# Kernel optimization log

Measured on AMD Instinct MI355X. Metric: run time of the kernel, lower is better.

## Reference

```python
import jax, jax.numpy as jnp
import numpy as np

N = 50000      # nodes
E = 800000     # edges (avg degree 16)
D = 128        # d_model
H = 8          # num_heads
DK = D // H    # d_k = 16


def setup_inputs() -> dict:
    key = jax.random.key(0)
    ks = jax.random.split(key, 9)
    scale = np.float32(1.0 / np.sqrt(D))
    return {
        "q": jax.random.normal(ks[0], (N, D), jnp.float32),
        "k": jax.random.normal(ks[1], (N, D), jnp.float32),
        "v": jax.random.normal(ks[2], (N, D), jnp.float32),
        "e": jax.random.normal(ks[3], (E, D), jnp.float32),
        "src": jax.random.randint(ks[4], (E,), 0, N),
        "dst": jax.random.randint(ks[5], (E,), 0, N),
        # nn.Linear(D, D, bias=False) weights, stored as [in, out]
        "Wq": jax.random.normal(ks[6], (D, D), jnp.float32) * scale,
        "Wk": jax.random.normal(ks[7], (D, D), jnp.float32) * scale,
        "Wv": jax.random.normal(ks[8], (D, D), jnp.float32) * scale,
    }


def reference(q, k, v, e, src, dst, Wq, Wk, Wv):
    inv_sqrt_dk = np.float32(1.0 / np.sqrt(DK))
    # node-level V projection, then per-edge gather of src V  -> [E, H, DK]
    Vn = (v @ Wv).reshape(N, H, DK)
    Ve = Vn[src]
    # per-edge Q from dst node, K from (src k + edge feature e)
    Qe = (q[dst] @ Wq).reshape(E, H, DK)
    Ke = ((k[src] + e) @ Wk).reshape(E, H, DK)
    # per-edge HxH score matrix: Q @ K^T / sqrt(d_k), leaky-relu
    s = jnp.einsum("ehd,egd->ehg", Qe, Ke) * inv_sqrt_dk   # [E, H, H]
    s = jax.nn.leaky_relu(s)
    # softmax over last head axis (within each edge, as in reduce_func dim=-1)
    A = jax.nn.softmax(s, axis=-1)
    # per-edge message, heads regrouped -> [E, D]
    He = jnp.einsum("ehg,egd->ehd", A, Ve).reshape(E, D)
    # plain sum over incoming edges per destination node -> [N, D]
    return jax.ops.segment_sum(He, dst, num_segments=N)
```

## Files before the change

kernel.cpp:

```cpp
#include <hip/hip_runtime.h>
#include <hip/hip_bf16.h>
#include <math.h>

#define NN 50000
#define EE 800000
#define DD 128
#define HH 8
#define DKK 16

typedef __attribute__((ext_vector_type(8))) short short8;
typedef __attribute__((ext_vector_type(4))) float f32x4;
typedef __attribute__((ext_vector_type(4))) unsigned short ushort4v;
typedef __attribute__((ext_vector_type(8))) unsigned short ushort8v;

static __device__ __forceinline__ unsigned short f2bf(float x) {
  __hip_bfloat16 h = __float2bfloat16(x);
  return *reinterpret_cast<unsigned short*>(&h);
}
static __device__ __forceinline__ float bf2f(unsigned short u) {
  return __uint_as_float(((unsigned int)u) << 16);
}

__global__ __launch_bounds__(256) void hist_kernel(const int* __restrict__ dst,
                                                   int* __restrict__ cnt) {
  int i4 = blockIdx.x * 256 + threadIdx.x;
  if (i4 < EE / 4) {
    int4 d = *(const int4*)&dst[i4 * 4];
    atomicAdd(&cnt[d.x], 1);
    atomicAdd(&cnt[d.y], 1);
    atomicAdd(&cnt[d.z], 1);
    atomicAdd(&cnt[d.w], 1);
  }
}

#define SCAN_NB ((NN + 1023) / 1024)

__global__ __launch_bounds__(256) void scan1_kernel(const int* __restrict__ cnt,
                                                    int* __restrict__ bsum) {
  __shared__ int red[256];
  const int b = blockIdx.x, t = threadIdx.x;
  const int base = b * 1024 + t * 4;
  int s = 0;
  if (base + 3 < NN) {
    int4 v = *(const int4*)&cnt[base];
    s = v.x + v.y + v.z + v.w;
  } else {
    for (int j = 0; j < 4; ++j) if (base + j < NN) s += cnt[base + j];
  }
  red[t] = s;
  __syncthreads();
  for (int off = 1; off < 256; off <<= 1) {
    int v = (t >= off) ? red[t - off] : 0;
    __syncthreads();
    red[t] += v;
    __syncthreads();
  }
  if (t == 255) bsum[b] = red[255];
}

__global__ __launch_bounds__(64) void scan2_kernel(const int* __restrict__ bsum,
                                                   int* __restrict__ bpre) {
  int t = threadIdx.x;
  int v = (t < SCAN_NB) ? bsum[t] : 0;
  for (int off = 1; off < 64; off <<= 1) {
    int u = __shfl_up(v, off);
    if (t >= off) v += u;
  }
  if (t < SCAN_NB) bpre[t + 1] = v;
  if (t == 0) bpre[0] = 0;
}

__global__ __launch_bounds__(256) void scan3_kernel(const int* __restrict__ cnt,
                                                    const int* __restrict__ bpre,
                                                    int* __restrict__ rowptr) {
  __shared__ int red[256];
  const int b = blockIdx.x, t = threadIdx.x;
  const int base = b * 1024 + t * 4;
  int v0 = 0, v1 = 0, v2 = 0, v3 = 0;
  if (base + 3 < NN) {
    int4 v = *(const int4*)&cnt[base];
    v0 = v.x; v1 = v.y; v2 = v.z; v3 = v.w;
  } else {
    if (base + 0 < NN) v0 = cnt[base + 0];
    if (base + 1 < NN) v1 = cnt[base + 1];
    if (base + 2 < NN) v2 = cnt[base + 2];
    if (base + 3 < NN) v3 = cnt[base + 3];
  }
  red[t] = v0 + v1 + v2 + v3;
  __syncthreads();
  for (int off = 1; off < 256; off <<= 1) {
    int v = (t >= off) ? red[t - off] : 0;
    __syncthreads();
    red[t] += v;
    __syncthreads();
  }
  int r = bpre[b] + ((t == 0) ? 0 : red[t - 1]);
  if (base + 0 < NN) { rowptr[base + 0] = r; r += v0; }
  if (base + 1 < NN) { rowptr[base + 1] = r; r += v1; }
  if (base + 2 < NN) { rowptr[base + 2] = r; r += v2; }
  if (base + 3 < NN) { rowptr[base + 3] = r; }
}

__global__ __launch_bounds__(256) void fill_kernel(const int* __restrict__ dst,
                                                   const int* __restrict__ rowptr,
                                                   int* __restrict__ cur,
                                                   int* __restrict__ perm) {
  int i4 = blockIdx.x * 256 + threadIdx.x;
  if (i4 < EE / 4) {
    int4 dv = *(const int4*)&dst[i4 * 4];
    int d0 = dv.x, d1 = dv.y, d2 = dv.z, d3 = dv.w;
    int s0 = atomicAdd(&cur[d0], 1); perm[rowptr[d0] + s0] = i4 * 4 + 0;
    int s1 = atomicAdd(&cur[d1], 1); perm[rowptr[d1] + s1] = i4 * 4 + 1;
    int s2 = atomicAdd(&cur[d2], 1); perm[rowptr[d2] + s2] = i4 * 4 + 2;
    int s3 = atomicAdd(&cur[d3], 1); perm[rowptr[d3] + s3] = i4 * 4 + 3;
  }
}

__global__ void prep_w_kernel(const float* __restrict__ Wq,
                              const float* __restrict__ Wk,
                              const float* __restrict__ Wv,
                              unsigned short* __restrict__ WqT,
                              unsigned short* __restrict__ WkT,
                              unsigned short* __restrict__ WvT) {
  int c = blockIdx.x & 127;
  int m = blockIdx.x >> 7;
  int j = threadIdx.x;
  const float* W = (m == 0) ? Wq : (m == 1) ? Wk : Wv;
  unsigned short* o = (m == 0) ? WqT : (m == 1) ? WkT : WvT;
  o[j * DD + c] = f2bf(W[c * DD + j]);
}

__global__ __launch_bounds__(512) void node_proj_kernel(
    const float* __restrict__ q, const float* __restrict__ v,
    const float* __restrict__ k,
    const unsigned short* __restrict__ WqT, const unsigned short* __restrict__ WvT,
    unsigned short* __restrict__ Qh, unsigned short* __restrict__ Vh,
    unsigned short* __restrict__ kh)
{
  __shared__ __align__(16) unsigned short xl[64 * 136];
  const int tid = threadIdx.x;
  const int n0 = blockIdx.x * 64;

  #pragma unroll
  for (int p = 0; p < 2; ++p) {
    int f = p * 512 + tid;
    int i = f >> 4, c8 = f & 15;
    int n = n0 + i;
    if (n < NN) {
      float4 a = *(const float4*)&k[(size_t)n * DD + c8 * 8];
      float4 b = *(const float4*)&k[(size_t)n * DD + c8 * 8 + 4];
      ushort8v o = { f2bf(a.x), f2bf(a.y), f2bf(a.z), f2bf(a.w),
                     f2bf(b.x), f2bf(b.y), f2bf(b.z), f2bf(b.w) };
      *(ushort8v*)&kh[(size_t)n * DD + c8 * 8] = o;
    }
  }

  for (int m = 0; m < 2; ++m) {
    const float* x = m ? v : q;
    const unsigned short* WT = m ? WvT : WqT;
    unsigned short* o = m ? Vh : Qh;

    __syncthreads();
    #pragma unroll
    for (int p = 0; p < 4; ++p) {
      int f = p * 512 + tid;
      int i = f >> 5, c4 = f & 31;
      int n = n0 + i;
      float4 t = (n < NN) ? *(const float4*)&x[(size_t)n * DD + c4 * 4]
                          : float4{0.f, 0.f, 0.f, 0.f};
      ushort4v u = { f2bf(t.x), f2bf(t.y), f2bf(t.z), f2bf(t.w) };
      *(ushort4v*)&xl[i * 136 + c4 * 4] = u;
    }
    __syncthreads();

    const int lane = tid & 63, wid = tid >> 6;
    const int rg = wid & 3, cg = wid >> 2;
    const int lr = lane & 15, lg = lane >> 4;

    f32x4 acc0 = {0.f,0.f,0.f,0.f}, acc1 = {0.f,0.f,0.f,0.f};
    f32x4 acc2 = {0.f,0.f,0.f,0.f}, acc3 = {0.f,0.f,0.f,0.f};

    const unsigned short* Ab = &xl[(rg * 16 + lr) * 136];
    const unsigned short* B0 = &WT[(size_t)(cg * 64 +  0 + lr) * DD];
    const unsigned short* B1 = &WT[(size_t)(cg * 64 + 16 + lr) * DD];
    const unsigned short* B2 = &WT[(size_t)(cg * 64 + 32 + lr) * DD];
    const unsigned short* B3 = &WT[(size_t)(cg * 64 + 48 + lr) * DD];

    #pragma unroll
    for (int kk = 0; kk < 4; ++kk) {
      const int kof = kk * 32 + lg * 8;
      short8 a = *(const short8*)(Ab + kof);
      acc0 = __builtin_amdgcn_mfma_f32_16x16x32_bf16(a, *(const short8*)(B0 + kof), acc0, 0, 0, 0);
      acc1 = __builtin_amdgcn_mfma_f32_16x16x32_bf16(a, *(const short8*)(B1 + kof), acc1, 0, 0, 0);
      acc2 = __builtin_amdgcn_mfma_f32_16x16x32_bf16(a, *(const short8*)(B2 + kof), acc2, 0, 0, 0);
      acc3 = __builtin_amdgcn_mfma_f32_16x16x32_bf16(a, *(const short8*)(B3 + kof), acc3, 0, 0, 0);
    }

    const int r0 = rg * 16 + lg * 4;
    const int cb = cg * 64 + lr;
    #pragma unroll
    for (int r = 0; r < 4; ++r) {
      int n = n0 + r0 + r;
      if (n < NN) {
        unsigned short* orow = &o[(size_t)n * DD + cb];
        orow[ 0] = f2bf(acc0[r]);
        orow[16] = f2bf(acc1[r]);
        orow[32] = f2bf(acc2[r]);
        orow[48] = f2bf(acc3[r]);
      }
    }
  }
}

__global__ __launch_bounds__(512) void edge_attn_kernel(
    const unsigned short* __restrict__ kh, const float* __restrict__ e,
    const int* __restrict__ src, const int* __restrict__ dst,
    const int* __restrict__ perm,
    const unsigned short* __restrict__ WkT,
    const unsigned short* __restrict__ Qh, const unsigned short* __restrict__ Vh,
    float* __restrict__ out)
{
  __shared__ __align__(16) unsigned short buf[128 * 136];
  __shared__ __align__(16) unsigned short vbuf[128 * 136];
  __shared__ __align__(16) unsigned short pbuf[8 * 16 * 24];
  __shared__ int s_perm[128], s_src[128], s_dst[128];

  const int tid = threadIdx.x;
  const size_t e0 = (size_t)blockIdx.x * 128;

  if (tid < 128) {
    int pe = perm[e0 + tid];
    s_perm[tid] = pe;
    s_src[tid] = src[pe];
    s_dst[tid] = dst[pe];
  }
  __syncthreads();

  #pragma unroll
  for (int p = 0; p < 4; ++p) {
    int f = p * 512 + tid;
    int i2 = f >> 4, c8 = f & 15;
    *(ushort8v*)&vbuf[i2 * 136 + c8 * 8] =
        *(const ushort8v*)&Vh[(size_t)s_src[i2] * DD + c8 * 8];
  }

  #pragma unroll
  for (int p = 0; p < 4; ++p) {
    int f = p * 512 + tid;
    int i2 = f >> 4, c8 = f & 15;
    ushort8v kv = *(const ushort8v*)&kh[(size_t)s_src[i2] * DD + c8 * 8];
    float4 ea = *(const float4*)&e[(size_t)s_perm[i2] * DD + c8 * 8];
    float4 eb = *(const float4*)&e[(size_t)s_perm[i2] * DD + c8 * 8 + 4];
    ushort8v o;
    o[0] = f2bf(bf2f(kv[0]) + ea.x);
    o[1] = f2bf(bf2f(kv[1]) + ea.y);
    o[2] = f2bf(bf2f(kv[2]) + ea.z);
    o[3] = f2bf(bf2f(kv[3]) + ea.w);
    o[4] = f2bf(bf2f(kv[4]) + eb.x);
    o[5] = f2bf(bf2f(kv[5]) + eb.y);
    o[6] = f2bf(bf2f(kv[6]) + eb.z);
    o[7] = f2bf(bf2f(kv[7]) + eb.w);
    *(ushort8v*)&buf[i2 * 136 + c8 * 8] = o;
  }
  __syncthreads();

  const int lane = tid & 63, wid = tid >> 6;
  const int lr = lane & 15, lg = lane >> 4;

  {
    const int rgA = wid & 3, rgB = (wid & 3) + 4, cg = wid >> 2;

    f32x4 aA0 = {0.f,0.f,0.f,0.f}, aA1 = {0.f,0.f,0.f,0.f};
    f32x4 aA2 = {0.f,0.f,0.f,0.f}, aA3 = {0.f,0.f,0.f,0.f};
    f32x4 aB0 = {0.f,0.f,0.f,0.f}, aB1 = {0.f,0.f,0.f,0.f};
    f32x4 aB2 = {0.f,0.f,0.f,0.f}, aB3 = {0.f,0.f,0.f,0.f};

    const unsigned short* AbA = &buf[(rgA * 16 + lr) * 136];
    const unsigned short* AbB = &buf[(rgB * 16 + lr) * 136];
    const unsigned short* B0 = &WkT[(size_t)(cg * 64 +  0 + lr) * DD];
    const unsigned short* B1 = &WkT[(size_t)(cg * 64 + 16 + lr) * DD];
    const unsigned short* B2 = &WkT[(size_t)(cg * 64 + 32 + lr) * DD];
    const unsigned short* B3 = &WkT[(size_t)(cg * 64 + 48 + lr) * DD];

    #pragma unroll
    for (int kk = 0; kk < 4; ++kk) {
      const int kof = kk * 32 + lg * 8;
      short8 b0 = *(const short8*)(B0 + kof);
      short8 b1 = *(const short8*)(B1 + kof);
      short8 b2 = *(const short8*)(B2 + kof);
      short8 b3 = *(const short8*)(B3 + kof);
      short8 fA = *(const short8*)(AbA + kof);
      short8 fB = *(const short8*)(AbB + kof);
      aA0 = __builtin_amdgcn_mfma_f32_16x16x32_bf16(fA, b0, aA0, 0, 0, 0);
      aA1 = __builtin_amdgcn_mfma_f32_16x16x32_bf16(fA, b1, aA1, 0, 0, 0);
      aA2 = __builtin_amdgcn_mfma_f32_16x16x32_bf16(fA, b2, aA2, 0, 0, 0);
      aA3 = __builtin_amdgcn_mfma_f32_16x16x32_bf16(fA, b3, aA3, 0, 0, 0);
      aB0 = __builtin_amdgcn_mfma_f32_16x16x32_bf16(fB, b0, aB0, 0, 0, 0);
      aB1 = __builtin_amdgcn_mfma_f32_16x16x32_bf16(fB, b1, aB1, 0, 0, 0);
      aB2 = __builtin_amdgcn_mfma_f32_16x16x32_bf16(fB, b2, aB2, 0, 0, 0);
      aB3 = __builtin_amdgcn_mfma_f32_16x16x32_bf16(fB, b3, aB3, 0, 0, 0);
    }

    __syncthreads();

    const int rA = rgA * 16 + lg * 4;
    const int rB = rgB * 16 + lg * 4;
    const int cb = cg * 64 + lr;
    #pragma unroll
    for (int r = 0; r < 4; ++r) {
      buf[(rA + r) * 136 + cb +  0] = f2bf(aA0[r]);
      buf[(rA + r) * 136 + cb + 16] = f2bf(aA1[r]);
      buf[(rA + r) * 136 + cb + 32] = f2bf(aA2[r]);
      buf[(rA + r) * 136 + cb + 48] = f2bf(aA3[r]);
      buf[(rB + r) * 136 + cb +  0] = f2bf(aB0[r]);
      buf[(rB + r) * 136 + cb + 16] = f2bf(aB1[r]);
      buf[(rB + r) * 136 + cb + 32] = f2bf(aB2[r]);
      buf[(rB + r) * 136 + cb + 48] = f2bf(aB3[r]);
    }
  }
  __syncthreads();

  {
    const int ebase = wid * 16;
    const bool valid = ((lr < 8) == (lg < 2));
    unsigned short* pb = &pbuf[wid * 16 * 24];
    const short8 zero8 = {0, 0, 0, 0, 0, 0, 0, 0};

    short8 qf[8];
    #pragma unroll
    for (int j = 0; j < 8; ++j) {
      if (lg < 2) {
        int ie = ebase + 2 * j + (lr >> 3);
        qf[j] = *(const short8*)&Qh[(size_t)s_dst[ie] * DD + (lr & 7) * DKK + lg * 8];
      } else qf[j] = zero8;
    }

    #pragma unroll
    for (int j = 0; j < 8; ++j) {
      const int iea = ebase + 2 * j, ieb = iea + 1;

      short8 af = zero8;
      if (lg < 2) {
        int ie = (lr < 8) ? iea : ieb;
        af = *(const short8*)&buf[ie * 136 + (lr & 7) * DKK + lg * 8];
      }
      f32x4 c = {0.f, 0.f, 0.f, 0.f};
      c = __builtin_amdgcn_mfma_f32_16x16x32_bf16(af, qf[j], c, 0, 0, 0);

      float s0, s1, s2, s3;
      {
        float x0 = c[0] * 0.25f, x1 = c[1] * 0.25f;
        float x2 = c[2] * 0.25f, x3 = c[3] * 0.25f;
        x0 = (x0 >= 0.f) ? x0 : 0.01f * x0;
        x1 = (x1 >= 0.f) ? x1 : 0.01f * x1;
        x2 = (x2 >= 0.f) ? x2 : 0.01f * x2;
        x3 = (x3 >= 0.f) ? x3 : 0.01f * x3;
        s0 = valid ? x0 : -1e30f;
        s1 = valid ? x1 : -1e30f;
        s2 = valid ? x2 : -1e30f;
        s3 = valid ? x3 : -1e30f;
      }
      float m = fmaxf(fmaxf(s0, s1), fmaxf(s2, s3));
      m = fmaxf(m, __shfl_xor(m, 16));
      m = fmaxf(m, __shfl_xor(m, 32));
      float p0 = __expf(s0 - m), p1 = __expf(s1 - m);
      float p2 = __expf(s2 - m), p3 = __expf(s3 - m);
      float su = p0 + p1 + p2 + p3;
      su += __shfl_xor(su, 16);
      su += __shfl_xor(su, 32);
      float rs = 1.0f / su;

      ushort4v pk = { f2bf(p0 * rs), f2bf(p1 * rs), f2bf(p2 * rs), f2bf(p3 * rs) };
      *(ushort4v*)&pb[lr * 24 + lg * 4] = pk;

      short8 pa = zero8;
      if (lg < 2) pa = *(const short8*)&pb[lr * 24 + lg * 8];
      short8 vf = zero8;
      if (lg < 2) {
        const unsigned short* vr = &vbuf[(lg ? ieb : iea) * 136 + lr];
        vf[0] = (short)vr[0 * 16];
        vf[1] = (short)vr[1 * 16];
        vf[2] = (short)vr[2 * 16];
        vf[3] = (short)vr[3 * 16];
        vf[4] = (short)vr[4 * 16];
        vf[5] = (short)vr[5 * 16];
        vf[6] = (short)vr[6 * 16];
        vf[7] = (short)vr[7 * 16];
      }
      f32x4 hc = {0.f, 0.f, 0.f, 0.f};
      hc = __builtin_amdgcn_mfma_f32_16x16x32_bf16(pa, vf, hc, 0, 0, 0);

      #pragma unroll
      for (int r = 0; r < 4; ++r) {
        int rr = lg * 4 + r;
        int ie = (rr < 8) ? iea : ieb;
        buf[ie * 136 + (rr & 7) * DKK + lr] = f2bf(hc[r]);
      }
    }
  }

  {
    const int c = tid >> 6, d2 = tid & 63;
    const int base = c * 16;
    float s0 = 0.0f, s1 = 0.0f;
    int curd = s_dst[base];
    #pragma unroll 8
    for (int j = 0; j < 16; ++j) {
      int i2 = base + j;
      int dn2 = s_dst[i2];
      if (dn2 != curd) {
        atomicAdd(&out[(size_t)curd * DD + d2 * 2],     s0);
        atomicAdd(&out[(size_t)curd * DD + d2 * 2 + 1], s1);
        s0 = 0.0f; s1 = 0.0f;
        curd = dn2;
      }
      unsigned int w = *(const unsigned int*)&buf[i2 * 136 + d2 * 2];
      s0 += bf2f((unsigned short)(w & 0xffff));
      s1 += bf2f((unsigned short)(w >> 16));
    }
    atomicAdd(&out[(size_t)curd * DD + d2 * 2],     s0);
    atomicAdd(&out[(size_t)curd * DD + d2 * 2 + 1], s1);
  }
}

extern "C" void kernel_launch(void* const* d_in, const int* in_sizes, int n_in,
                              void* d_out, int out_size, void* d_ws, size_t ws_size,
                              hipStream_t stream) {
  const float* q  = (const float*)d_in[0];
  const float* k  = (const float*)d_in[1];
  const float* v  = (const float*)d_in[2];
  const float* e  = (const float*)d_in[3];
  const int*   src = (const int*)d_in[4];
  const int*   dst = (const int*)d_in[5];
  const float* Wq = (const float*)d_in[6];
  const float* Wk = (const float*)d_in[7];
  const float* Wv = (const float*)d_in[8];

  float* out = (float*)d_out;
  char* wsb = (char*)d_ws;
  unsigned short* Qh  = (unsigned short*)wsb;
  unsigned short* Vh  = Qh + (size_t)NN * DD;
  unsigned short* kh  = Vh + (size_t)NN * DD;
  unsigned short* WqT = kh + (size_t)NN * DD;
  unsigned short* WkT = WqT + DD * DD;
  unsigned short* WvT = WkT + DD * DD;
  int* cnt    = (int*)(WvT + DD * DD);
  int* cur    = cnt + NN;
  int* rowptr = cur + NN;
  int* bsum   = rowptr + NN + 1;
  int* bpre   = bsum + 64;
  int* perm   = bpre + 64;

  hipMemsetAsync(d_out, 0, (size_t)NN * DD * sizeof(float), stream);
  hipMemsetAsync(cnt, 0, 2 * NN * sizeof(int), stream);

  hist_kernel <<<(EE / 4 + 255) / 256, 256, 0, stream>>>(dst, cnt);
  scan1_kernel<<<SCAN_NB, 256, 0, stream>>>(cnt, bsum);
  scan2_kernel<<<1, 64, 0, stream>>>(bsum, bpre);
  scan3_kernel<<<SCAN_NB, 256, 0, stream>>>(cnt, bpre, rowptr);
  fill_kernel <<<(EE / 4 + 255) / 256, 256, 0, stream>>>(dst, rowptr, cur, perm);

  prep_w_kernel<<<3 * DD, DD, 0, stream>>>(Wq, Wk, Wv, WqT, WkT, WvT);
  node_proj_kernel<<<(NN + 63) / 64, 512, 0, stream>>>(q, v, k, WqT, WvT,
                                                       Qh, Vh, kh);
  edge_attn_kernel<<<EE / 128, 512, 0, stream>>>(kh, e, src, dst, perm,
                                                 WkT, Qh, Vh, out);
}
```

Before: 387.3 us.

## Make edge attention kernel wave-private to eliminate block-wide barriers

Restructures the edge attention kernel so each wavefront owns 16 edges end to end: it loads its own indices, gathers K+e and V rows into a private LDS slice, does the full 16x128 Wk projection itself with 8 MFMA accumulators, and then runs attention and aggregation. This removes all __syncthreads calls and the cross-wave split of the projection GEMM, so waves no longer wait on each other. The LDS row padding is also dropped from 136 to 128, which can cause bank conflicts on the strided column accesses. Each wave now reads all of WkT from global or cache instead of a quarter, and it relies on wave-level ordering of LDS writes and reads without explicit barriers.

New measurement: 475.1 us. 1.23x slower.

```diff
diff --git a/kernel.cpp b/kernel.cpp
--- a/kernel.cpp
+++ b/kernel.cpp
@@ -220,37 +220,41 @@
     const unsigned short* __restrict__ Qh, const unsigned short* __restrict__ Vh,
     float* __restrict__ out)
 {
-  __shared__ __align__(16) unsigned short buf[128 * 136];
-  __shared__ __align__(16) unsigned short vbuf[128 * 136];
+  __shared__ __align__(16) unsigned short buf[128 * 128];
+  __shared__ __align__(16) unsigned short vbuf[128 * 128];
   __shared__ __align__(16) unsigned short pbuf[8 * 16 * 24];
   __shared__ int s_perm[128], s_src[128], s_dst[128];
 
   const int tid = threadIdx.x;
-  const size_t e0 = (size_t)blockIdx.x * 128;
-
-  if (tid < 128) {
-    int pe = perm[e0 + tid];
-    s_perm[tid] = pe;
-    s_src[tid] = src[pe];
-    s_dst[tid] = dst[pe];
-  }
-  __syncthreads();
+  const int lane = tid & 63, wid = tid >> 6;
+  const int lr = lane & 15, lg = lane >> 4;
+  const int ebase = blockIdx.x * 128 + wid * 16;
+
+  unsigned short* bw = &buf[wid * 16 * 128];
+  unsigned short* vw = &vbuf[wid * 16 * 128];
+  unsigned short* pb = &pbuf[wid * 16 * 24];
+  int* sp = &s_perm[wid * 16];
+  int* ss = &s_src[wid * 16];
+  int* sd = &s_dst[wid * 16];
+
+  if (lane < 16) {
+    int pe = perm[ebase + lane];
+    sp[lane] = pe;
+    ss[lane] = src[pe];
+    sd[lane] = dst[pe];
+  }
 
   #pragma unroll
   for (int p = 0; p < 4; ++p) {
-    int f = p * 512 + tid;
-    int i2 = f >> 4, c8 = f & 15;
-    *(ushort8v*)&vbuf[i2 * 136 + c8 * 8] =
-        *(const ushort8v*)&Vh[(size_t)s_src[i2] * DD + c8 * 8];
-  }
-
-  #pragma unroll
-  for (int p = 0; p < 4; ++p) {
-    int f = p * 512 + tid;
-    int i2 = f >> 4, c8 = f & 15;
-    ushort8v kv = *(const ushort8v*)&kh[(size_t)s_src[i2] * DD + c8 * 8];
-    float4 ea = *(const float4*)&e[(size_t)s_perm[i2] * DD + c8 * 8];
-    float4 eb = *(const float4*)&e[(size_t)s_perm[i2] * DD + c8 * 8 + 4];
+    const int row = p * 4 + lg;
+    const int sn = ss[row];
+    ushort8v vv = *(const ushort8v*)&Vh[(size_t)sn * DD + lr * 8];
+    *(ushort8v*)&vw[row * 128 + lr * 8] = vv;
+
+    ushort8v kv = *(const ushort8v*)&kh[(size_t)sn * DD + lr * 8];
+    const float* ep = &e[(size_t)sp[row] * DD + lr * 8];
+    float4 ea = *(const float4*)ep;
+    float4 eb = *(const float4*)(ep + 4);
     ushort8v o;
     o[0] = f2bf(bf2f(kv[0]) + ea.x);
     o[1] = f2bf(bf2f(kv[1]) + ea.y);
@@ -260,89 +264,53 @@
     o[5] = f2bf(bf2f(kv[5]) + eb.y);
     o[6] = f2bf(bf2f(kv[6]) + eb.z);
     o[7] = f2bf(bf2f(kv[7]) + eb.w);
-    *(ushort8v*)&buf[i2 * 136 + c8 * 8] = o;
-  }
-  __syncthreads();
-
-  const int lane = tid & 63, wid = tid >> 6;
-  const int lr = lane & 15, lg = lane >> 4;
+    *(ushort8v*)&bw[row * 128 + lr * 8] = o;
+  }
 
   {
-    const int rgA = wid & 3, rgB = (wid & 3) + 4, cg = wid >> 2;
-
-    f32x4 aA0 = {0.f,0.f,0.f,0.f}, aA1 = {0.f,0.f,0.f,0.f};
-    f32x4 aA2 = {0.f,0.f,0.f,0.f}, aA3 = {0.f,0.f,0.f,0.f};
-    f32x4 aB0 = {0.f,0.f,0.f,0.f}, aB1 = {0.f,0.f,0.f,0.f};
-    f32x4 aB2 = {0.f,0.f,0.f,0.f}, aB3 = {0.f,0.f,0.f,0.f};
-
-    const unsigned short* AbA = &buf[(rgA * 16 + lr) * 136];
-    const unsigned short* AbB = &buf[(rgB * 16 + lr) * 136];
-    const unsigned short* B0 = &WkT[(size_t)(cg * 64 +  0 + lr) * DD];
-    const unsigned short* B1 = &WkT[(size_t)(cg * 64 + 16 + lr) * DD];
-    const unsigned short* B2 = &WkT[(size_t)(cg * 64 + 32 + lr) * DD];
-    const unsigned short* B3 = &WkT[(size_t)(cg * 64 + 48 + lr) * DD];
-
+    f32x4 acc[8];
+    #pragma unroll
+    for (int c = 0; c < 8; ++c) acc[c] = f32x4{0.f, 0.f, 0.f, 0.f};
+
+    const unsigned short* Ab = &bw[lr * 128];
     #pragma unroll
     for (int kk = 0; kk < 4; ++kk) {
       const int kof = kk * 32 + lg * 8;
-      short8 b0 = *(const short8*)(B0 + kof);
-      short8 b1 = *(const short8*)(B1 + kof);
-      short8 b2 = *(const short8*)(B2 + kof);
-      short8 b3 = *(const short8*)(B3 + kof);
-      short8 fA = *(const short8*)(AbA + kof);
-      short8 fB = *(const short8*)(AbB + kof);
-      aA0 = __builtin_amdgcn_mfma_f32_16x16x32_bf16(fA, b0, aA0, 0, 0, 0);
-      aA1 = __builtin_amdgcn_mfma_f32_16x16x32_bf16(fA, b1, aA1, 0, 0, 0);
-      aA2 = __builtin_amdgcn_mfma_f32_16x16x32_bf16(fA, b2, aA2, 0, 0, 0);
-      aA3 = __builtin_amdgcn_mfma_f32_16x16x32_bf16(fA, b3, aA3, 0, 0, 0);
-      aB0 = __builtin_amdgcn_mfma_f32_16x16x32_bf16(fB, b0, aB0, 0, 0, 0);
-      aB1 = __builtin_amdgcn_mfma_f32_16x16x32_bf16(fB, b1, aB1, 0, 0, 0);
-      aB2 = __builtin_amdgcn_mfma_f32_16x16x32_bf16(fB, b2, aB2, 0, 0, 0);
-      aB3 = __builtin_amdgcn_mfma_f32_16x16x32_bf16(fB, b3, aB3, 0, 0, 0);
-    }
-
-    __syncthreads();
-
-    const int rA = rgA * 16 + lg * 4;
-    const int rB = rgB * 16 + lg * 4;
-    const int cb = cg * 64 + lr;
-    #pragma unroll
-    for (int r = 0; r < 4; ++r) {
-      buf[(rA + r) * 136 + cb +  0] = f2bf(aA0[r]);
-      buf[(rA + r) * 136 + cb + 16] = f2bf(aA1[r]);
-      buf[(rA + r) * 136 + cb + 32] = f2bf(aA2[r]);
-      buf[(rA + r) * 136 + cb + 48] = f2bf(aA3[r]);
-      buf[(rB + r) * 136 + cb +  0] = f2bf(aB0[r]);
-      buf[(rB + r) * 136 + cb + 16] = f2bf(aB1[r]);
-      buf[(rB + r) * 136 + cb + 32] = f2bf(aB2[r]);
-      buf[(rB + r) * 136 + cb + 48] = f2bf(aB3[r]);
-    }
-  }
-  __syncthreads();
+      short8 a = *(const short8*)(Ab + kof);
+      #pragma unroll
+      for (int c = 0; c < 8; ++c) {
+        short8 b = *(const short8*)&WkT[(size_t)(c * 16 + lr) * DD + kof];
+        acc[c] = __builtin_amdgcn_mfma_f32_16x16x32_bf16(a, b, acc[c], 0, 0, 0);
+      }
+    }
+    #pragma unroll
+    for (int c = 0; c < 8; ++c)
+      #pragma unroll
+      for (int r = 0; r < 4; ++r)
+        bw[(lg * 4 + r) * 128 + c * 16 + lr] = f2bf(acc[c][r]);
+  }
 
   {
-    const int ebase = wid * 16;
     const bool valid = ((lr < 8) == (lg < 2));
-    unsigned short* pb = &pbuf[wid * 16 * 24];
     const short8 zero8 = {0, 0, 0, 0, 0, 0, 0, 0};
 
     short8 qf[8];
     #pragma unroll
     for (int j = 0; j < 8; ++j) {
       if (lg < 2) {
-        int ie = ebase + 2 * j + (lr >> 3);
-        qf[j] = *(const short8*)&Qh[(size_t)s_dst[ie] * DD + (lr & 7) * DKK + lg * 8];
+        int ie = 2 * j + (lr >> 3);
+        qf[j] = *(const short8*)&Qh[(size_t)sd[ie] * DD + (lr & 7) * DKK + lg * 8];
       } else qf[j] = zero8;
     }
 
     #pragma unroll
     for (int j = 0; j < 8; ++j) {
-      const int iea = ebase + 2 * j, ieb = iea + 1;
+      const int iea = 2 * j, ieb = iea + 1;
 
       short8 af = zero8;
       if (lg < 2) {
         int ie = (lr < 8) ? iea : ieb;
-        af = *(const short8*)&buf[ie * 136 + (lr & 7) * DKK + lg * 8];
+        af = *(const short8*)&bw[ie * 128 + (lr & 7) * DKK + lg * 8];
       }
       f32x4 c = {0.f, 0.f, 0.f, 0.f};
       c = __builtin_amdgcn_mfma_f32_16x16x32_bf16(af, qf[j], c, 0, 0, 0);
@@ -377,7 +345,7 @@
       if (lg < 2) pa = *(const short8*)&pb[lr * 24 + lg * 8];
       short8 vf = zero8;
       if (lg < 2) {
-        const unsigned short* vr = &vbuf[(lg ? ieb : iea) * 136 + lr];
+        const unsigned short* vr = &vw[(lg ? ieb : iea) * 128 + lr];
         vf[0] = (short)vr[0 * 16];
         vf[1] = (short)vr[1 * 16];
         vf[2] = (short)vr[2 * 16];
@@ -394,27 +362,25 @@
       for (int r = 0; r < 4; ++r) {
         int rr = lg * 4 + r;
         int ie = (rr < 8) ? iea : ieb;
-        buf[ie * 136 + (rr & 7) * DKK + lr] = f2bf(hc[r]);
+        bw[ie * 128 + (rr & 7) * DKK + lr] = f2bf(hc[r]);
       }
     }
   }
 
   {
-    const int c = tid >> 6, d2 = tid & 63;
-    const int base = c * 16;
+    const int d2 = lane;
     float s0 = 0.0f, s1 = 0.0f;
-    int curd = s_dst[base];
+    int curd = sd[0];
     #pragma unroll 8
     for (int j = 0; j < 16; ++j) {
-      int i2 = base + j;
-      int dn2 = s_dst[i2];
+      int dn2 = sd[j];
       if (dn2 != curd) {
         atomicAdd(&out[(size_t)curd * DD + d2 * 2],     s0);
         atomicAdd(&out[(size_t)curd * DD + d2 * 2 + 1], s1);
         s0 = 0.0f; s1 = 0.0f;
         curd = dn2;
       }
-      unsigned int w = *(const unsigned int*)&buf[i2 * 136 + d2 * 2];
+      unsigned int w = *(const unsigned int*)&bw[j * 128 + d2 * 2];
       s0 += bf2f((unsigned short)(w & 0xffff));
       s1 += bf2f((unsigned short)(w >> 16));
     }
```

## Batch edge gathers into registers, hoist Q loads, fold scan2 into scan3

Applied to the files above, without the earlier changes.

Removes the separate scan2 kernel launch: each scan3 block loads the block sums into shared memory and computes its own prefix serially. In the edge attention kernel, all V, K, e and Q global gathers are issued together into registers before any shared-memory writes, so more loads are in flight. A launch-bounds occupancy hint of 4 is also added. The cost is higher register pressure, which may cause spills under the occupancy hint.

Result: no change. 384.5 us (-0.7%).

```diff
diff --git a/kernel.cpp b/kernel.cpp
--- a/kernel.cpp
+++ b/kernel.cpp
@@ -58,23 +58,13 @@
   if (t == 255) bsum[b] = red[255];
 }
 
-__global__ __launch_bounds__(64) void scan2_kernel(const int* __restrict__ bsum,
-                                                   int* __restrict__ bpre) {
-  int t = threadIdx.x;
-  int v = (t < SCAN_NB) ? bsum[t] : 0;
-  for (int off = 1; off < 64; off <<= 1) {
-    int u = __shfl_up(v, off);
-    if (t >= off) v += u;
-  }
-  if (t < SCAN_NB) bpre[t + 1] = v;
-  if (t == 0) bpre[0] = 0;
-}
-
 __global__ __launch_bounds__(256) void scan3_kernel(const int* __restrict__ cnt,
-                                                    const int* __restrict__ bpre,
+                                                    const int* __restrict__ bsum,
                                                     int* __restrict__ rowptr) {
   __shared__ int red[256];
+  __shared__ int bs[SCAN_NB];
   const int b = blockIdx.x, t = threadIdx.x;
+  if (t < SCAN_NB) bs[t] = bsum[t];
   const int base = b * 1024 + t * 4;
   int v0 = 0, v1 = 0, v2 = 0, v3 = 0;
   if (base + 3 < NN) {
@@ -94,7 +84,9 @@
     red[t] += v;
     __syncthreads();
   }
-  int r = bpre[b] + ((t == 0) ? 0 : red[t - 1]);
+  int bpre = 0;
+  for (int j = 0; j < b; ++j) bpre += bs[j];
+  int r = bpre + ((t == 0) ? 0 : red[t - 1]);
   if (base + 0 < NN) { rowptr[base + 0] = r; r += v0; }
   if (base + 1 < NN) { rowptr[base + 1] = r; r += v1; }
   if (base + 2 < NN) { rowptr[base + 2] = r; r += v2; }
@@ -212,7 +204,7 @@
   }
 }
 
-__global__ __launch_bounds__(512) void edge_attn_kernel(
+__global__ __launch_bounds__(512, 4) void edge_attn_kernel(
     const unsigned short* __restrict__ kh, const float* __restrict__ e,
     const int* __restrict__ src, const int* __restrict__ dst,
     const int* __restrict__ perm,
@@ -227,6 +219,8 @@
 
   const int tid = threadIdx.x;
   const size_t e0 = (size_t)blockIdx.x * 128;
+  const int lane = tid & 63, wid = tid >> 6;
+  const int lr = lane & 15, lg = lane >> 4;
 
   if (tid < 128) {
     int pe = perm[e0 + tid];
@@ -236,36 +230,47 @@
   }
   __syncthreads();
 
+  ushort8v vv[4], kv[4];
+  float4 ea[4], eb[4];
   #pragma unroll
   for (int p = 0; p < 4; ++p) {
     int f = p * 512 + tid;
     int i2 = f >> 4, c8 = f & 15;
-    *(ushort8v*)&vbuf[i2 * 136 + c8 * 8] =
-        *(const ushort8v*)&Vh[(size_t)s_src[i2] * DD + c8 * 8];
+    vv[p] = *(const ushort8v*)&Vh[(size_t)s_src[i2] * DD + c8 * 8];
+    kv[p] = *(const ushort8v*)&kh[(size_t)s_src[i2] * DD + c8 * 8];
+    const float* ep = &e[(size_t)s_perm[i2] * DD + c8 * 8];
+    ea[p] = *(const float4*)ep;
+    eb[p] = *(const float4*)(ep + 4);
+  }
+
+  const short8 zero8 = {0, 0, 0, 0, 0, 0, 0, 0};
+  const int ebase = wid * 16;
+  short8 qf[8];
+  #pragma unroll
+  for (int j = 0; j < 8; ++j) {
+    if (lg < 2) {
+      int ie = ebase + 2 * j + (lr >> 3);
+      qf[j] = *(const short8*)&Qh[(size_t)s_dst[ie] * DD + (lr & 7) * DKK + lg * 8];
+    } else qf[j] = zero8;
   }
 
   #pragma unroll
   for (int p = 0; p < 4; ++p) {
     int f = p * 512 + tid;
     int i2 = f >> 4, c8 = f & 15;
-    ushort8v kv = *(const ushort8v*)&kh[(size_t)s_src[i2] * DD + c8 * 8];
-    float4 ea = *(const float4*)&e[(size_t)s_perm[i2] * DD + c8 * 8];
-    float4 eb = *(const float4*)&e[(size_t)s_perm[i2] * DD + c8 * 8 + 4];
+    *(ushort8v*)&vbuf[i2 * 136 + c8 * 8] = vv[p];
     ushort8v o;
-    o[0] = f2bf(bf2f(kv[0]) + ea.x);
-    o[1] = f2bf(bf2f(kv[1]) + ea.y);
-    o[2] = f2bf(bf2f(kv[2]) + ea.z);
-    o[3] = f2bf(bf2f(kv[3]) + ea.w);
-    o[4] = f2bf(bf2f(kv[4]) + eb.x);
-    o[5] = f2bf(bf2f(kv[5]) + eb.y);
-    o[6] = f2bf(bf2f(kv[6]) + eb.z);
-    o[7] = f2bf(bf2f(kv[7]) + eb.w);
+    o[0] = f2bf(bf2f(kv[p][0]) + ea[p].x);
+    o[1] = f2bf(bf2f(kv[p][1]) + ea[p].y);
+    o[2] = f2bf(bf2f(kv[p][2]) + ea[p].z);
+    o[3] = f2bf(bf2f(kv[p][3]) + ea[p].w);
+    o[4] = f2bf(bf2f(kv[p][4]) + eb[p].x);
+    o[5] = f2bf(bf2f(kv[p][5]) + eb[p].y);
+    o[6] = f2bf(bf2f(kv[p][6]) + eb[p].z);
+    o[7] = f2bf(bf2f(kv[p][7]) + eb[p].w);
     *(ushort8v*)&buf[i2 * 136 + c8 * 8] = o;
   }
   __syncthreads();
-
-  const int lane = tid & 63, wid = tid >> 6;
-  const int lr = lane & 15, lg = lane >> 4;
 
   {
     const int rgA = wid & 3, rgB = (wid & 3) + 4, cg = wid >> 2;
@@ -321,19 +326,8 @@
   __syncthreads();
 
   {
-    const int ebase = wid * 16;
     const bool valid = ((lr < 8) == (lg < 2));
     unsigned short* pb = &pbuf[wid * 16 * 24];
-    const short8 zero8 = {0, 0, 0, 0, 0, 0, 0, 0};
-
-    short8 qf[8];
-    #pragma unroll
-    for (int j = 0; j < 8; ++j) {
-      if (lg < 2) {
-        int ie = ebase + 2 * j + (lr >> 3);
-        qf[j] = *(const short8*)&Qh[(size_t)s_dst[ie] * DD + (lr & 7) * DKK + lg * 8];
-      } else qf[j] = zero8;
-    }
 
     #pragma unroll
     for (int j = 0; j < 8; ++j) {
@@ -400,8 +394,8 @@
   }
 
   {
-    const int c = tid >> 6, d2 = tid & 63;
-    const int base = c * 16;
+    const int d2 = lane;
+    const int base = ebase;
     float s0 = 0.0f, s1 = 0.0f;
     int curd = s_dst[base];
     #pragma unroll 8
@@ -448,16 +442,14 @@
   int* cur    = cnt + NN;
   int* rowptr = cur + NN;
   int* bsum   = rowptr + NN + 1;
-  int* bpre   = bsum + 64;
-  int* perm   = bpre + 64;
+  int* perm   = bsum + 64;
 
   hipMemsetAsync(d_out, 0, (size_t)NN * DD * sizeof(float), stream);
   hipMemsetAsync(cnt, 0, 2 * NN * sizeof(int), stream);
 
   hist_kernel <<<(EE / 4 + 255) / 256, 256, 0, stream>>>(dst, cnt);
   scan1_kernel<<<SCAN_NB, 256, 0, stream>>>(cnt, bsum);
-  scan2_kernel<<<1, 64, 0, stream>>>(bsum, bpre);
-  scan3_kernel<<<SCAN_NB, 256, 0, stream>>>(cnt, bpre, rowptr);
+  scan3_kernel<<<SCAN_NB, 256, 0, stream>>>(cnt, bsum, rowptr);
   fill_kernel <<<(EE / 4 + 255) / 256, 256, 0, stream>>>(dst, rowptr, cur, perm);
 
   prep_w_kernel<<<3 * DD, DD, 0, stream>>>(Wq, Wk, Wv, WqT, WkT, WvT);
```
